# Kernel optimization log

Hardware: AMD Instinct MI355X
Metric: run time of the kernel (lower is better)

The kernel has to match this reference:

```python
import jax, jax.numpy as jnp
import numpy as np

B, S, H, D = 2, 2048, 16, 64
HID = H * D
NEG_INF = -10000.0

def setup_inputs() -> dict:
    key = jax.random.key(0)
    ks = jax.random.split(key, 4)
    std = 0.02
    return {
        'x': jax.random.normal(ks[0], (B, S, HID), dtype=jnp.float32),
        'mask': jnp.ones((B, S), dtype=jnp.int32),
        'Wq': jax.random.normal(ks[1], (HID, HID), dtype=jnp.float32) * std,
        'bq': jnp.zeros((HID,), dtype=jnp.float32),
        'Wk': jax.random.normal(ks[2], (HID, HID), dtype=jnp.float32) * std,
        'bk': jnp.zeros((HID,), dtype=jnp.float32),
        'Wv': jax.random.normal(ks[3], (HID, HID), dtype=jnp.float32) * std,
        'bv': jnp.zeros((HID,), dtype=jnp.float32),
    }

def reference(x, mask, Wq, bq, Wk, bk, Wv, bv):
    b, s, _ = x.shape
    def split_heads(t):  # [b,s,HID] -> [b,H,s,D]
        return t.reshape(b, s, H, D).transpose(0, 2, 1, 3)
    q = split_heads(x @ Wq + bq)
    k = split_heads(x @ Wk + bk)
    v = split_heads(x @ Wv + bv)
    scores = jnp.einsum('bhqd,bhkd->bhqk', q, k) / jnp.sqrt(jnp.float32(D))
    # additive padding mask: [b,1,1,s] broadcast over query positions and heads
    adder = (1.0 - mask.astype(scores.dtype))[:, None, None, :] * NEG_INF
    probs = jax.nn.softmax(scores + adder, axis=-1)
    ctx = jnp.einsum('bhqk,bhkd->bhqd', probs, v)  # [b,H,s,D]
    return ctx.transpose(0, 2, 1, 3).reshape(b, s, HID)
```

## Files before the change

### kernel.cpp

```cpp
#include <hip/hip_runtime.h>
#include <cstddef>

constexpr int Bc = 2, Sc = 2048, Hc = 16, Dc = 64, HIDc = 1024;
#define NEG_INF -10000.0f

typedef _Float16 half8  __attribute__((ext_vector_type(8)));
typedef _Float16 half4  __attribute__((ext_vector_type(4)));
typedef float   floatx4 __attribute__((ext_vector_type(4)));

__global__ __launch_bounds__(256) void cvt_x_kernel(const float* __restrict__ x,
                                                    _Float16* __restrict__ xh) {
    int i = (blockIdx.x * 256 + threadIdx.x) * 8;
    float4 a = *(const float4*)(x + i);
    float4 b = *(const float4*)(x + i + 4);
    half8 h;
    h[0] = (_Float16)a.x; h[1] = (_Float16)a.y; h[2] = (_Float16)a.z; h[3] = (_Float16)a.w;
    h[4] = (_Float16)b.x; h[5] = (_Float16)b.y; h[6] = (_Float16)b.z; h[7] = (_Float16)b.w;
    *(half8*)(xh + i) = h;
}

__global__ __launch_bounds__(256) void cvt_w_kernel(const float* __restrict__ Wq,
                                                    const float* __restrict__ Wk,
                                                    const float* __restrict__ Wv,
                                                    _Float16* __restrict__ Wt) {
    const float* W = (blockIdx.z == 0) ? Wq : (blockIdx.z == 1) ? Wk : Wv;
    _Float16* out = Wt + (size_t)blockIdx.z * HIDc * HIDc;
    __shared__ _Float16 T[64][65];
    const int t = threadIdx.x;
    const int kb = blockIdx.x * 64, nb = blockIdx.y * 64;
    const int r = t >> 2, c4 = (t & 3) * 16;
    #pragma unroll
    for (int i = 0; i < 16; i += 4) {
        float4 a = *(const float4*)(W + (size_t)(kb + r) * HIDc + nb + c4 + i);
        T[c4 + i + 0][r] = (_Float16)a.x;
        T[c4 + i + 1][r] = (_Float16)a.y;
        T[c4 + i + 2][r] = (_Float16)a.z;
        T[c4 + i + 3][r] = (_Float16)a.w;
    }
    __syncthreads();
    const int n = t >> 2, k4 = (t & 3) * 16;
    half8 o0, o1;
    #pragma unroll
    for (int j = 0; j < 8; ++j) { o0[j] = T[n][k4 + j]; o1[j] = T[n][k4 + 8 + j]; }
    *(half8*)(out + (size_t)(nb + n) * HIDc + kb + k4)     = o0;
    *(half8*)(out + (size_t)(nb + n) * HIDc + kb + k4 + 8) = o1;
}

#define PSTR 40
__global__ __launch_bounds__(256, 2) void proj_kernel(
    const _Float16* __restrict__ xh, const _Float16* __restrict__ Wt,
    const float* __restrict__ bq, const float* __restrict__ bk, const float* __restrict__ bv,
    _Float16* __restrict__ qw, _Float16* __restrict__ kw, _Float16* __restrict__ vt)
{
    const int z = blockIdx.z;
    const _Float16* Wz = Wt + (size_t)z * HIDc * HIDc;
    const float* bias = (z == 0) ? bq : (z == 1) ? bk : bv;

    __shared__ _Float16 As[2][128 * PSTR];
    __shared__ _Float16 Bs[2][128 * PSTR];

    const int t = threadIdx.x;
    const int lane = t & 63, w = t >> 6;
    const int quad = lane >> 4, l16 = lane & 15;
    const int m0 = blockIdx.y * 128, n0 = blockIdx.x * 128;
    const int wm = (w >> 1) * 64, wn = (w & 1) * 64;
    const int sr = t >> 1, sh = (t & 1) * 16;

    floatx4 acc[4][4];
    #pragma unroll
    for (int mb = 0; mb < 4; ++mb)
        #pragma unroll
        for (int nb = 0; nb < 4; ++nb) acc[mb][nb] = floatx4{0.f, 0.f, 0.f, 0.f};

    {
        const _Float16* ap = xh + (size_t)(m0 + sr) * HIDc + sh;
        const _Float16* bp = Wz + (size_t)(n0 + sr) * HIDc + sh;
        *(uint4*)(As[0] + sr * PSTR + sh)     = *(const uint4*)(ap);
        *(uint4*)(As[0] + sr * PSTR + sh + 8) = *(const uint4*)(ap + 8);
        *(uint4*)(Bs[0] + sr * PSTR + sh)     = *(const uint4*)(bp);
        *(uint4*)(Bs[0] + sr * PSTR + sh + 8) = *(const uint4*)(bp + 8);
    }
    __syncthreads();

    #pragma unroll 2
    for (int it = 0; it < HIDc / 32; ++it) {
        const int cur = it & 1;
        const int kn = (it + 1 < HIDc / 32) ? (it + 1) * 32 : 0;
        const _Float16* ap = xh + (size_t)(m0 + sr) * HIDc + kn + sh;
        const _Float16* bp = Wz + (size_t)(n0 + sr) * HIDc + kn + sh;
        uint4 a0 = *(const uint4*)(ap);
        uint4 a1 = *(const uint4*)(ap + 8);
        uint4 b0 = *(const uint4*)(bp);
        uint4 b1 = *(const uint4*)(bp + 8);

        half8 af[4], bf[4];
        #pragma unroll
        for (int mb = 0; mb < 4; ++mb)
            af[mb] = *(const half8*)(As[cur] + (wm + mb * 16 + l16) * PSTR + quad * 8);
        #pragma unroll
        for (int nb = 0; nb < 4; ++nb)
            bf[nb] = *(const half8*)(Bs[cur] + (wn + nb * 16 + l16) * PSTR + quad * 8);
        #pragma unroll
        for (int mb = 0; mb < 4; ++mb)
            #pragma unroll
            for (int nb = 0; nb < 4; ++nb)
                acc[mb][nb] = __builtin_amdgcn_mfma_f32_16x16x32_f16(
                    af[mb], bf[nb], acc[mb][nb], 0, 0, 0);

        *(uint4*)(As[cur ^ 1] + sr * PSTR + sh)     = a0;
        *(uint4*)(As[cur ^ 1] + sr * PSTR + sh + 8) = a1;
        *(uint4*)(Bs[cur ^ 1] + sr * PSTR + sh)     = b0;
        *(uint4*)(Bs[cur ^ 1] + sr * PSTR + sh + 8) = b1;
        __syncthreads();
    }

    #pragma unroll
    for (int nb = 0; nb < 4; ++nb) {
        const int N = n0 + wn + nb * 16 + l16;
        const float bi = bias[N];
        const int h = N >> 6, d = N & 63;
        #pragma unroll
        for (int mb = 0; mb < 4; ++mb) {
            #pragma unroll
            for (int r = 0; r < 4; ++r) {
                const int M = m0 + wm + mb * 16 + quad * 4 + r;
                const int bI = M >> 11, s = M & (Sc - 1);
                const float v = acc[mb][nb][r] + bi;
                if (z == 0)
                    qw[(((size_t)(bI * Hc + h)) * Sc + s) * Dc + d] = (_Float16)(v * 0.125f);
                else if (z == 1)
                    kw[(((size_t)(bI * Hc + h)) * Sc + s) * Dc + d] = (_Float16)v;
                else
                    vt[(((size_t)(bI * Hc + h)) * Dc + d) * Sc + s] = (_Float16)v;
            }
        }
    }
}

__global__ __launch_bounds__(256, 2) void attn_kernel(
    const _Float16* __restrict__ qw, const _Float16* __restrict__ kw,
    const _Float16* __restrict__ vt, const int* __restrict__ mask,
    float* __restrict__ out)
{
    __shared__ float adder[Sc];
    __shared__ __align__(16) _Float16 Ks[2][64][72];
    __shared__ __align__(16) _Float16 Vs[2][64][72];

    const int t = threadIdx.x;
    const int lane = t & 63, w = t >> 6;
    const int quad = lane >> 4, l16 = lane & 15;
    const int bh = blockIdx.y;
    const int bI = bh >> 4, h = bh & 15;

    const _Float16* Qp = qw + (size_t)bh * Sc * Dc;
    const _Float16* Kp = kw + (size_t)bh * Sc * Dc;
    const _Float16* Vp = vt + (size_t)bh * Dc * Sc;

    const int srow = t >> 3;
    const int scol = (t & 7) * 8;

    {
        const int4* mp = (const int4*)(mask + bI * Sc);
        #pragma unroll
        for (int i = 0; i < 2; ++i) {
            int4 m4 = mp[t * 2 + i];
            int base = (t * 2 + i) * 4;
            adder[base + 0] = (1.0f - (float)m4.x) * NEG_INF;
            adder[base + 1] = (1.0f - (float)m4.y) * NEG_INF;
            adder[base + 2] = (1.0f - (float)m4.z) * NEG_INF;
            adder[base + 3] = (1.0f - (float)m4.w) * NEG_INF;
        }
    }
    #pragma unroll
    for (int hf = 0; hf < 2; ++hf) {
        const int row = srow + 32 * hf;
        uint4 kv = *(const uint4*)(Kp + (size_t)row * Dc + scol);
        uint4 vv = *(const uint4*)(Vp + (size_t)row * Sc + scol);
        *(uint4*)(&Ks[0][row][scol]) = kv;
        *(uint4*)(&Vs[0][row][scol]) = vv;
    }

    const int qrow = blockIdx.x * 128 + w * 32;
    half8 aq[2][2];
    #pragma unroll
    for (int s = 0; s < 2; ++s)
        #pragma unroll
        for (int hh = 0; hh < 2; ++hh)
            aq[s][hh] = *(const half8*)(Qp + (size_t)(qrow + 16 * s + l16) * Dc
                                        + hh * 32 + quad * 8);

    floatx4 o[2][4];
    #pragma unroll
    for (int s = 0; s < 2; ++s)
        #pragma unroll
        for (int db = 0; db < 4; ++db) o[s][db] = floatx4{0.f, 0.f, 0.f, 0.f};
    float lsum[2] = {0.f, 0.f};

    __syncthreads();

    #pragma unroll 2
    for (int it = 0; it < Sc / 64; ++it) {
        const int cur = it & 1;
        const int kt = it * 64;
        const int ktn = (it + 1 < Sc / 64) ? kt + 64 : 0;
        uint4 kstg[2], vstg[2];
        #pragma unroll
        for (int hf = 0; hf < 2; ++hf) {
            const int row = srow + 32 * hf;
            kstg[hf] = *(const uint4*)(Kp + (size_t)(ktn + row) * Dc + scol);
            vstg[hf] = *(const uint4*)(Vp + (size_t)row * Sc + ktn + scol);
        }

        half8 kb[4][2];
        half4 vb[4][4];
        #pragma unroll
        for (int nb = 0; nb < 4; ++nb)
            #pragma unroll
            for (int hh = 0; hh < 2; ++hh)
                kb[nb][hh] = *(const half8*)(&Ks[cur][nb * 16 + l16][hh * 32 + quad * 8]);
        #pragma unroll
        for (int nb = 0; nb < 4; ++nb)
            #pragma unroll
            for (int db = 0; db < 4; ++db)
                vb[nb][db] = *(const half4*)(&Vs[cur][db * 16 + l16][nb * 16 + quad * 4]);

        floatx4 st[2][4];
        #pragma unroll
        for (int s = 0; s < 2; ++s)
            #pragma unroll
            for (int nb = 0; nb < 4; ++nb) {
                floatx4 acc = floatx4{0.f, 0.f, 0.f, 0.f};
                acc = __builtin_amdgcn_mfma_f32_16x16x32_f16(kb[nb][0], aq[s][0], acc, 0, 0, 0);
                acc = __builtin_amdgcn_mfma_f32_16x16x32_f16(kb[nb][1], aq[s][1], acc, 0, 0, 0);
                st[s][nb] = acc;
            }

        half4 pa[2][4];
        #pragma unroll
        for (int nb = 0; nb < 4; ++nb) {
            const float4 a4 = *(const float4*)&adder[kt + nb * 16 + quad * 4];
            const float ad[4] = {a4.x, a4.y, a4.z, a4.w};
            #pragma unroll
            for (int s = 0; s < 2; ++s)
                #pragma unroll
                for (int r = 0; r < 4; ++r) {
                    const float p = __expf(st[s][nb][r] + ad[r]);
                    lsum[s] += p;
                    pa[s][nb][r] = (_Float16)p;
                }
        }

        #pragma unroll
        for (int s = 0; s < 2; ++s)
            #pragma unroll
            for (int nb = 0; nb < 4; ++nb)
                #pragma unroll
                for (int db = 0; db < 4; ++db)
                    o[s][db] = __builtin_amdgcn_mfma_f32_16x16x16f16(
                        pa[s][nb], vb[nb][db], o[s][db], 0, 0, 0);

        #pragma unroll
        for (int hf = 0; hf < 2; ++hf) {
            const int row = srow + 32 * hf;
            *(uint4*)(&Ks[cur ^ 1][row][scol]) = kstg[hf];
            *(uint4*)(&Vs[cur ^ 1][row][scol]) = vstg[hf];
        }
        __syncthreads();
    }

    #pragma unroll
    for (int s = 0; s < 2; ++s) {
        lsum[s] += __shfl_xor(lsum[s], 16, 64);
        lsum[s] += __shfl_xor(lsum[s], 32, 64);
    }
    float* op = out + (size_t)bI * Sc * HIDc + h * Dc;
    #pragma unroll
    for (int s = 0; s < 2; ++s)
        #pragma unroll
        for (int r = 0; r < 4; ++r) {
            const float inv = 1.0f / __shfl(lsum[s], quad * 4 + r, 64);
            const int q = qrow + 16 * s + quad * 4 + r;
            #pragma unroll
            for (int db = 0; db < 4; ++db)
                op[(size_t)q * HIDc + db * 16 + l16] = o[s][db][r] * inv;
        }
}

extern "C" void kernel_launch(void* const* d_in, const int* in_sizes, int n_in,
                              void* d_out, int out_size, void* d_ws, size_t ws_size,
                              hipStream_t stream) {
    const float* x    = (const float*)d_in[0];
    const int*   mask = (const int*)  d_in[1];
    const float* Wq   = (const float*)d_in[2];
    const float* bq   = (const float*)d_in[3];
    const float* Wk   = (const float*)d_in[4];
    const float* bk   = (const float*)d_in[5];
    const float* Wv   = (const float*)d_in[6];
    const float* bv   = (const float*)d_in[7];
    float* out = (float*)d_out;

    char* ws = (char*)d_ws;
    _Float16* xh = (_Float16*)(ws);
    _Float16* Wt = (_Float16*)(ws + (size_t)8  * 1024 * 1024);
    _Float16* qw = (_Float16*)(ws + (size_t)14 * 1024 * 1024);
    _Float16* kw = (_Float16*)(ws + (size_t)22 * 1024 * 1024);
    _Float16* vt = (_Float16*)(ws + (size_t)30 * 1024 * 1024);

    cvt_x_kernel<<<(Bc * Sc * HIDc) / (256 * 8), 256, 0, stream>>>(x, xh);
    cvt_w_kernel<<<dim3(HIDc / 64, HIDc / 64, 3), 256, 0, stream>>>(Wq, Wk, Wv, Wt);
    proj_kernel<<<dim3(HIDc / 128, (Bc * Sc) / 128, 3), 256, 0, stream>>>(
        xh, Wt, bq, bk, bv, qw, kw, vt);
    attn_kernel<<<dim3(Sc / 128, Bc * Hc), 256, 0, stream>>>(qw, kw, vt, mask, out);
}
```

Measured before the change: 188.5 us.

## Split attention over key range with combine pass, merge conversion kernels

Attention now uses 128-thread blocks of 64 query rows with 32-key tiles. When the workspace is large enough it splits the key range in two across blockIdx.z, writes unnormalized partial outputs and row sums, and a new combine kernel adds and normalizes them. The x and weight fp16 conversions are merged into one launch that also precomputes the mask adder in global memory, so the attention kernel no longer builds it in shared memory. This raises block count and occupancy on the attention stage, at the cost of an extra kernel and 32MB of partial-output traffic. Summing partials without a per-split max is valid only because the softmax here is computed without max subtraction, as before.

```diff
diff --git a/kernel.cpp b/kernel.cpp
--- a/kernel.cpp
+++ b/kernel.cpp
@@ -8,42 +8,64 @@
 typedef _Float16 half4  __attribute__((ext_vector_type(4)));
 typedef float   floatx4 __attribute__((ext_vector_type(4)));
 
-__global__ __launch_bounds__(256) void cvt_x_kernel(const float* __restrict__ x,
-                                                    _Float16* __restrict__ xh) {
-    int i = (blockIdx.x * 256 + threadIdx.x) * 8;
-    float4 a = *(const float4*)(x + i);
-    float4 b = *(const float4*)(x + i + 4);
-    half8 h;
-    h[0] = (_Float16)a.x; h[1] = (_Float16)a.y; h[2] = (_Float16)a.z; h[3] = (_Float16)a.w;
-    h[4] = (_Float16)b.x; h[5] = (_Float16)b.y; h[6] = (_Float16)b.z; h[7] = (_Float16)b.w;
-    *(half8*)(xh + i) = h;
-}
-
-__global__ __launch_bounds__(256) void cvt_w_kernel(const float* __restrict__ Wq,
-                                                    const float* __restrict__ Wk,
-                                                    const float* __restrict__ Wv,
-                                                    _Float16* __restrict__ Wt) {
-    const float* W = (blockIdx.z == 0) ? Wq : (blockIdx.z == 1) ? Wk : Wv;
-    _Float16* out = Wt + (size_t)blockIdx.z * HIDc * HIDc;
-    __shared__ _Float16 T[64][65];
+#define OFF_AD 0u
+#define OFF_XH (64u * 1024)
+#define OFF_WT (OFF_XH + 8u * 1024 * 1024)
+#define OFF_QW (OFF_WT + 6u * 1024 * 1024)
+#define OFF_KW (OFF_QW + 8u * 1024 * 1024)
+#define OFF_VT (OFF_KW + 8u * 1024 * 1024)
+#define OFF_PO (OFF_VT + 8u * 1024 * 1024)
+#define OFF_PL (OFF_PO + 32u * 1024 * 1024)
+#define WS_NEED ((size_t)OFF_PL + 512u * 1024)
+
+__global__ __launch_bounds__(256) void cvt_kernel(
+    const float* __restrict__ x, const int* __restrict__ mask,
+    const float* __restrict__ Wq, const float* __restrict__ Wk,
+    const float* __restrict__ Wv,
+    _Float16* __restrict__ xh, _Float16* __restrict__ Wt,
+    float* __restrict__ adder_g)
+{
     const int t = threadIdx.x;
-    const int kb = blockIdx.x * 64, nb = blockIdx.y * 64;
-    const int r = t >> 2, c4 = (t & 3) * 16;
-    #pragma unroll
-    for (int i = 0; i < 16; i += 4) {
-        float4 a = *(const float4*)(W + (size_t)(kb + r) * HIDc + nb + c4 + i);
-        T[c4 + i + 0][r] = (_Float16)a.x;
-        T[c4 + i + 1][r] = (_Float16)a.y;
-        T[c4 + i + 2][r] = (_Float16)a.z;
-        T[c4 + i + 3][r] = (_Float16)a.w;
-    }
-    __syncthreads();
-    const int n = t >> 2, k4 = (t & 3) * 16;
-    half8 o0, o1;
-    #pragma unroll
-    for (int j = 0; j < 8; ++j) { o0[j] = T[n][k4 + j]; o1[j] = T[n][k4 + 8 + j]; }
-    *(half8*)(out + (size_t)(nb + n) * HIDc + kb + k4)     = o0;
-    *(half8*)(out + (size_t)(nb + n) * HIDc + kb + k4 + 8) = o1;
+    const int z = blockIdx.z;
+    if (z < 3) {
+        const float* W = (z == 0) ? Wq : (z == 1) ? Wk : Wv;
+        _Float16* out = Wt + (size_t)z * HIDc * HIDc;
+        __shared__ _Float16 T[64][65];
+        const int kb = blockIdx.x * 64, nb = blockIdx.y * 64;
+        const int r = t >> 2, c4 = (t & 3) * 16;
+        #pragma unroll
+        for (int i = 0; i < 16; i += 4) {
+            float4 a = *(const float4*)(W + (size_t)(kb + r) * HIDc + nb + c4 + i);
+            T[c4 + i + 0][r] = (_Float16)a.x;
+            T[c4 + i + 1][r] = (_Float16)a.y;
+            T[c4 + i + 2][r] = (_Float16)a.z;
+            T[c4 + i + 3][r] = (_Float16)a.w;
+        }
+        __syncthreads();
+        const int n = t >> 2, k4 = (t & 3) * 16;
+        half8 o0, o1;
+        #pragma unroll
+        for (int j = 0; j < 8; ++j) { o0[j] = T[n][k4 + j]; o1[j] = T[n][k4 + 8 + j]; }
+        *(half8*)(out + (size_t)(nb + n) * HIDc + kb + k4)     = o0;
+        *(half8*)(out + (size_t)(nb + n) * HIDc + kb + k4 + 8) = o1;
+    } else {
+        const int cid = blockIdx.y * 16 + blockIdx.x;
+        const int base = cid * 16384;
+        #pragma unroll
+        for (int i = 0; i < 8; ++i) {
+            const int idx = base + i * 2048 + t * 8;
+            float4 a = *(const float4*)(x + idx);
+            float4 b = *(const float4*)(x + idx + 4);
+            half8 h;
+            h[0] = (_Float16)a.x; h[1] = (_Float16)a.y; h[2] = (_Float16)a.z; h[3] = (_Float16)a.w;
+            h[4] = (_Float16)b.x; h[5] = (_Float16)b.y; h[6] = (_Float16)b.z; h[7] = (_Float16)b.w;
+            *(half8*)(xh + idx) = h;
+        }
+        if (blockIdx.y == 0) {
+            const int idx = blockIdx.x * 256 + t;
+            adder_g[idx] = (1.0f - (float)mask[idx]) * NEG_INF;
+        }
+    }
 }
 
 #define PSTR 40
@@ -137,50 +159,44 @@
     }
 }
 
-__global__ __launch_bounds__(256, 2) void attn_kernel(
+__global__ __launch_bounds__(128, 3) void attn_kernel(
     const _Float16* __restrict__ qw, const _Float16* __restrict__ kw,
-    const _Float16* __restrict__ vt, const int* __restrict__ mask,
-    float* __restrict__ out)
+    const _Float16* __restrict__ vt, const float* __restrict__ adder_g,
+    float* __restrict__ part_o, float* __restrict__ part_l,
+    float* __restrict__ out, int nsplit)
 {
-    __shared__ float adder[Sc];
-    __shared__ __align__(16) _Float16 Ks[2][64][72];
-    __shared__ __align__(16) _Float16 Vs[2][64][72];
+    __shared__ __align__(16) _Float16 Ks[2][32][72];
+    __shared__ __align__(16) _Float16 Vs[2][64][40];
 
     const int t = threadIdx.x;
     const int lane = t & 63, w = t >> 6;
     const int quad = lane >> 4, l16 = lane & 15;
     const int bh = blockIdx.y;
     const int bI = bh >> 4, h = bh & 15;
+    const int half = blockIdx.z;
+    const int kt0 = half * (Sc / nsplit);
+    const int niter = (Sc / nsplit) / 32;
 
     const _Float16* Qp = qw + (size_t)bh * Sc * Dc;
     const _Float16* Kp = kw + (size_t)bh * Sc * Dc;
     const _Float16* Vp = vt + (size_t)bh * Dc * Sc;
-
-    const int srow = t >> 3;
-    const int scol = (t & 7) * 8;
+    const float* adp = adder_g + bI * Sc;
+
+    const int srK = t >> 2, scK = (t & 3) * 16;
+    const int srV = t >> 1, scV = (t & 1) * 16;
 
     {
-        const int4* mp = (const int4*)(mask + bI * Sc);
-        #pragma unroll
-        for (int i = 0; i < 2; ++i) {
-            int4 m4 = mp[t * 2 + i];
-            int base = (t * 2 + i) * 4;
-            adder[base + 0] = (1.0f - (float)m4.x) * NEG_INF;
-            adder[base + 1] = (1.0f - (float)m4.y) * NEG_INF;
-            adder[base + 2] = (1.0f - (float)m4.z) * NEG_INF;
-            adder[base + 3] = (1.0f - (float)m4.w) * NEG_INF;
-        }
-    }
-    #pragma unroll
-    for (int hf = 0; hf < 2; ++hf) {
-        const int row = srow + 32 * hf;
-        uint4 kv = *(const uint4*)(Kp + (size_t)row * Dc + scol);
-        uint4 vv = *(const uint4*)(Vp + (size_t)row * Sc + scol);
-        *(uint4*)(&Ks[0][row][scol]) = kv;
-        *(uint4*)(&Vs[0][row][scol]) = vv;
-    }
-
-    const int qrow = blockIdx.x * 128 + w * 32;
+        uint4 k0 = *(const uint4*)(Kp + (size_t)(kt0 + srK) * Dc + scK);
+        uint4 k1 = *(const uint4*)(Kp + (size_t)(kt0 + srK) * Dc + scK + 8);
+        uint4 v0 = *(const uint4*)(Vp + (size_t)srV * Sc + kt0 + scV);
+        uint4 v1 = *(const uint4*)(Vp + (size_t)srV * Sc + kt0 + scV + 8);
+        *(uint4*)(&Ks[0][srK][scK])     = k0;
+        *(uint4*)(&Ks[0][srK][scK + 8]) = k1;
+        *(uint4*)(&Vs[0][srV][scV])     = v0;
+        *(uint4*)(&Vs[0][srV][scV + 8]) = v1;
+    }
+
+    const int qrow = blockIdx.x * 64 + w * 32;
     half8 aq[2][2];
     #pragma unroll
     for (int s = 0; s < 2; ++s)
@@ -199,46 +215,43 @@
     __syncthreads();
 
     #pragma unroll 2
-    for (int it = 0; it < Sc / 64; ++it) {
+    for (int it = 0; it < niter; ++it) {
         const int cur = it & 1;
-        const int kt = it * 64;
-        const int ktn = (it + 1 < Sc / 64) ? kt + 64 : 0;
-        uint4 kstg[2], vstg[2];
-        #pragma unroll
-        for (int hf = 0; hf < 2; ++hf) {
-            const int row = srow + 32 * hf;
-            kstg[hf] = *(const uint4*)(Kp + (size_t)(ktn + row) * Dc + scol);
-            vstg[hf] = *(const uint4*)(Vp + (size_t)row * Sc + ktn + scol);
-        }
-
-        half8 kb[4][2];
-        half4 vb[4][4];
-        #pragma unroll
-        for (int nb = 0; nb < 4; ++nb)
+        const int kt = kt0 + it * 32;
+        const int ktn = (it + 1 < niter) ? kt + 32 : kt0;
+        uint4 k0 = *(const uint4*)(Kp + (size_t)(ktn + srK) * Dc + scK);
+        uint4 k1 = *(const uint4*)(Kp + (size_t)(ktn + srK) * Dc + scK + 8);
+        uint4 v0 = *(const uint4*)(Vp + (size_t)srV * Sc + ktn + scV);
+        uint4 v1 = *(const uint4*)(Vp + (size_t)srV * Sc + ktn + scV + 8);
+
+        half8 kb[2][2];
+        half4 vb[2][4];
+        #pragma unroll
+        for (int nb = 0; nb < 2; ++nb)
             #pragma unroll
             for (int hh = 0; hh < 2; ++hh)
                 kb[nb][hh] = *(const half8*)(&Ks[cur][nb * 16 + l16][hh * 32 + quad * 8]);
         #pragma unroll
-        for (int nb = 0; nb < 4; ++nb)
+        for (int nb = 0; nb < 2; ++nb)
             #pragma unroll
             for (int db = 0; db < 4; ++db)
                 vb[nb][db] = *(const half4*)(&Vs[cur][db * 16 + l16][nb * 16 + quad * 4]);
 
-        floatx4 st[2][4];
+        floatx4 st[2][2];
         #pragma unroll
         for (int s = 0; s < 2; ++s)
             #pragma unroll
-            for (int nb = 0; nb < 4; ++nb) {
+            for (int nb = 0; nb < 2; ++nb) {
                 floatx4 acc = floatx4{0.f, 0.f, 0.f, 0.f};
                 acc = __builtin_amdgcn_mfma_f32_16x16x32_f16(kb[nb][0], aq[s][0], acc, 0, 0, 0);
                 acc = __builtin_amdgcn_mfma_f32_16x16x32_f16(kb[nb][1], aq[s][1], acc, 0, 0, 0);
                 st[s][nb] = acc;
             }
 
-        half4 pa[2][4];
-        #pragma unroll
-        for (int nb = 0; nb < 4; ++nb) {
-            const float4 a4 = *(const float4*)&adder[kt + nb * 16 + quad * 4];
+        half4 pa[2][2];
+        #pragma unroll
+        for (int nb = 0; nb < 2; ++nb) {
+            const float4 a4 = *(const float4*)&adp[kt + nb * 16 + quad * 4];
             const float ad[4] = {a4.x, a4.y, a4.z, a4.w};
             #pragma unroll
             for (int s = 0; s < 2; ++s)
@@ -253,18 +266,16 @@
         #pragma unroll
         for (int s = 0; s < 2; ++s)
             #pragma unroll
-            for (int nb = 0; nb < 4; ++nb)
+            for (int nb = 0; nb < 2; ++nb)
                 #pragma unroll
                 for (int db = 0; db < 4; ++db)
                     o[s][db] = __builtin_amdgcn_mfma_f32_16x16x16f16(
                         pa[s][nb], vb[nb][db], o[s][db], 0, 0, 0);
 
-        #pragma unroll
-        for (int hf = 0; hf < 2; ++hf) {
-            const int row = srow + 32 * hf;
-            *(uint4*)(&Ks[cur ^ 1][row][scol]) = kstg[hf];
-            *(uint4*)(&Vs[cur ^ 1][row][scol]) = vstg[hf];
-        }
+        *(uint4*)(&Ks[cur ^ 1][srK][scK])     = k0;
+        *(uint4*)(&Ks[cur ^ 1][srK][scK + 8]) = k1;
+        *(uint4*)(&Vs[cur ^ 1][srV][scV])     = v0;
+        *(uint4*)(&Vs[cur ^ 1][srV][scV + 8]) = v1;
         __syncthreads();
     }
 
@@ -273,17 +284,60 @@
         lsum[s] += __shfl_xor(lsum[s], 16, 64);
         lsum[s] += __shfl_xor(lsum[s], 32, 64);
     }
-    float* op = out + (size_t)bI * Sc * HIDc + h * Dc;
-    #pragma unroll
-    for (int s = 0; s < 2; ++s)
-        #pragma unroll
-        for (int r = 0; r < 4; ++r) {
-            const float inv = 1.0f / __shfl(lsum[s], quad * 4 + r, 64);
-            const int q = qrow + 16 * s + quad * 4 + r;
-            #pragma unroll
-            for (int db = 0; db < 4; ++db)
-                op[(size_t)q * HIDc + db * 16 + l16] = o[s][db][r] * inv;
-        }
+
+    if (nsplit == 1) {
+        float* op = out + (size_t)bI * Sc * HIDc + h * Dc;
+        #pragma unroll
+        for (int s = 0; s < 2; ++s)
+            #pragma unroll
+            for (int r = 0; r < 4; ++r) {
+                const float inv = 1.0f / __shfl(lsum[s], quad * 4 + r, 64);
+                const int q = qrow + 16 * s + quad * 4 + r;
+                #pragma unroll
+                for (int db = 0; db < 4; ++db)
+                    op[(size_t)q * HIDc + db * 16 + l16] = o[s][db][r] * inv;
+            }
+    } else {
+        float* po = part_o + ((size_t)half * 32 + bh) * Sc * Dc;
+        #pragma unroll
+        for (int s = 0; s < 2; ++s)
+            #pragma unroll
+            for (int r = 0; r < 4; ++r) {
+                const int q = qrow + 16 * s + quad * 4 + r;
+                #pragma unroll
+                for (int db = 0; db < 4; ++db)
+                    po[(size_t)q * Dc + db * 16 + l16] = o[s][db][r];
+            }
+        if (quad == 0) {
+            #pragma unroll
+            for (int s = 0; s < 2; ++s)
+                part_l[((size_t)half * 32 + bh) * Sc + qrow + 16 * s + l16] = lsum[s];
+        }
+    }
+}
+
+__global__ __launch_bounds__(256) void combine_kernel(
+    const float* __restrict__ part_o, const float* __restrict__ part_l,
+    float* __restrict__ out)
+{
+    const int g = blockIdx.x * 256 + threadIdx.x;
+    const int d4 = g & 15;
+    const int q  = (g >> 4) & (Sc - 1);
+    const int bh = g >> 15;
+    const int bI = bh >> 4, h = bh & 15;
+    const float* poA = part_o + (size_t)bh * Sc * Dc + (size_t)q * Dc + d4 * 4;
+    const float* poB = poA + (size_t)32 * Sc * Dc;
+    const float lA = part_l[(size_t)bh * Sc + q];
+    const float lB = part_l[(size_t)32 * Sc + (size_t)bh * Sc + q];
+    const float inv = 1.0f / (lA + lB);
+    float4 a = *(const float4*)poA;
+    float4 b = *(const float4*)poB;
+    float4 r;
+    r.x = (a.x + b.x) * inv;
+    r.y = (a.y + b.y) * inv;
+    r.z = (a.z + b.z) * inv;
+    r.w = (a.w + b.w) * inv;
+    *(float4*)(out + (size_t)bI * Sc * HIDc + (size_t)q * HIDc + h * Dc + d4 * 4) = r;
 }
 
 extern "C" void kernel_launch(void* const* d_in, const int* in_sizes, int n_in,
@@ -300,15 +354,22 @@
     float* out = (float*)d_out;
 
     char* ws = (char*)d_ws;
-    _Float16* xh = (_Float16*)(ws);
-    _Float16* Wt = (_Float16*)(ws + (size_t)8  * 1024 * 1024);
-    _Float16* qw = (_Float16*)(ws + (size_t)14 * 1024 * 1024);
-    _Float16* kw = (_Float16*)(ws + (size_t)22 * 1024 * 1024);
-    _Float16* vt = (_Float16*)(ws + (size_t)30 * 1024 * 1024);
-
-    cvt_x_kernel<<<(Bc * Sc * HIDc) / (256 * 8), 256, 0, stream>>>(x, xh);
-    cvt_w_kernel<<<dim3(HIDc / 64, HIDc / 64, 3), 256, 0, stream>>>(Wq, Wk, Wv, Wt);
+    float*    adder = (float*)   (ws + OFF_AD);
+    _Float16* xh    = (_Float16*)(ws + OFF_XH);
+    _Float16* Wt    = (_Float16*)(ws + OFF_WT);
+    _Float16* qw    = (_Float16*)(ws + OFF_QW);
+    _Float16* kw    = (_Float16*)(ws + OFF_KW);
+    _Float16* vt    = (_Float16*)(ws + OFF_VT);
+    float*    po    = (float*)   (ws + OFF_PO);
+    float*    pl    = (float*)   (ws + OFF_PL);
+
+    const int nsplit = (ws_size >= WS_NEED) ? 2 : 1;
+
+    cvt_kernel<<<dim3(16, 16, 4), 256, 0, stream>>>(x, mask, Wq, Wk, Wv, xh, Wt, adder);
     proj_kernel<<<dim3(HIDc / 128, (Bc * Sc) / 128, 3), 256, 0, stream>>>(
         xh, Wt, bq, bk, bv, qw, kw, vt);
-    attn_kernel<<<dim3(Sc / 128, Bc * Hc), 256, 0, stream>>>(qw, kw, vt, mask, out);
-}
+    attn_kernel<<<dim3(Sc / 64, Bc * Hc, nsplit), 128, 0, stream>>>(
+        qw, kw, vt, adder, po, pl, out, nsplit);
+    if (nsplit == 2)
+        combine_kernel<<<(Bc * Hc * Sc * Dc / 4) / 256, 256, 0, stream>>>(po, pl, out);
+}
```

Result: slower. 204.1 us (+8.3%).
